# Kernel tuning notes

Measured on AMD Instinct MI355X. Metric: run time of the kernel, lower is better.

## Reference

```python
import jax, jax.numpy as jnp
import numpy as np

IN_DIM = 1024
MEM_DIM = 1024
T = 256
M = 512


def setup_inputs() -> dict:
    key = jax.random.key(0)
    ks = jax.random.split(key, 16)
    s = 0.02
    return {
        "inputs": jax.random.normal(ks[0], (T, 1, IN_DIM), jnp.float32),
        "hiddn_state_mat": jax.random.normal(ks[1], (M, MEM_DIM), jnp.float32),
        "W_ioux": jax.random.normal(ks[2], (IN_DIM, 3 * MEM_DIM), jnp.float32) * s,
        "b_ioux": jnp.zeros((3 * MEM_DIM,), jnp.float32),
        "W_iouh": jax.random.normal(ks[3], (MEM_DIM, 3 * MEM_DIM), jnp.float32) * s,
        "b_iouh": jnp.zeros((3 * MEM_DIM,), jnp.float32),
        "W_fx": jax.random.normal(ks[4], (IN_DIM, MEM_DIM), jnp.float32) * s,
        "b_fx": jnp.zeros((MEM_DIM,), jnp.float32),
        "W_fh": jax.random.normal(ks[5], (MEM_DIM, MEM_DIM), jnp.float32) * s,
        "b_fh": jnp.zeros((MEM_DIM,), jnp.float32),
        "Wa": jax.random.normal(ks[6], (1, MEM_DIM), jnp.float32) * 0.05,
        "W_attnh": jax.random.normal(ks[7], (2 * MEM_DIM, MEM_DIM), jnp.float32) * s,
        "b_attnh": jnp.zeros((MEM_DIM,), jnp.float32),
    }


def reference(inputs, hiddn_state_mat, W_ioux, b_ioux, W_iouh, b_iouh,
              W_fx, b_fx, W_fh, b_fh, Wa, W_attnh, b_attnh):
    m = W_fh.shape[1]
    n_rows = hiddn_state_mat.shape[0]

    def step(carry, x):
        c, h = carry  # [1, m] each; x: [1, in_dim]
        iou = x @ W_ioux + b_ioux + h @ W_iouh + b_iouh  # [1, 3m]
        i, o, u = jnp.split(iou, 3, axis=1)
        i = jax.nn.sigmoid(i); o = jax.nn.sigmoid(o); u = jnp.tanh(u)
        f = jax.nn.sigmoid(h @ W_fh + b_fh + x @ W_fx + b_fx)  # [1, m]
        c_new = i * u + f * c  # sum over the single child is identity
        h_new = o * jnp.tanh(c_new)  # [1, m]
        # attention over fixed hidden-state memory
        h_rep = jnp.broadcast_to(h_new, (n_rows, m))
        cat = jnp.concatenate([h_rep, hiddn_state_mat], axis=1)  # [M, 2m]
        t = jnp.tanh(cat @ W_attnh + b_attnh)  # [M, m]
        scores = t @ Wa[0]  # [M] == Wa @ t.T
        s = jax.nn.softmax(scores)[:, None]  # [M, 1]
        h_att = (jnp.sum((1.0 - s) * hiddn_state_mat, axis=0, keepdims=True)
                 + jnp.sum(s * h_rep, axis=0, keepdims=True))  # [1, m]
        return (c_new, h_att), h_att[0]

    init = (jnp.zeros((1, m), inputs.dtype), jnp.zeros((1, m), inputs.dtype))
    (_, _), h_all = jax.lax.scan(step, init, inputs)
    return h_all  # [T, mem_dim]; last row is the final child_h
```

## Files before the change

### kernel.cpp

```cpp
#include <hip/hip_runtime.h>
#include <hip/hip_bf16.h>

#define T_STEPS 256
#define MDIM 1024
#define MROWS 512
#define NBLK 128
#define GRID NBLK
#define NTHR 512

#define OFF_WGB     0u
#define OFF_WATT    2097152u
#define OFF_HPRET   3145728u
#define OFF_XIOU    3670016u
#define OFF_XF      4456448u
#define OFF_G       4718592u
#define OFF_HT      5767168u
#define OFF_HCOL    6291456u
#define OFF_HCOLW   6292480u
#define OFF_SCORED  6297600u
#define OFF_HLINE   6313984u

#define BIAS32  4294967296.0
#define SUBBIAS (16.0 * 4294967296.0)
#define DONE_TH (16.0 * 4294967296.0 - 1073741824.0)

typedef __attribute__((ext_vector_type(8))) short short8;
typedef __attribute__((ext_vector_type(4))) float f32x4;

__device__ inline float fast_tanh(float v) {
    float x = fminf(fmaxf(v, -15.f), 15.f);
    float z = __expf(2.f * x);
    return (z - 1.f) / (z + 1.f);
}
__device__ inline float sigm(float v) { return 1.f / (1.f + __expf(-v)); }

__device__ inline float wave_red(float v) {
#pragma unroll
    for (int s = 32; s > 0; s >>= 1) v += __shfl_down(v, s, 64);
    return v;
}

__device__ __host__ inline unsigned short f2b(float f) {
    __hip_bfloat16 h = __float2bfloat16(f);
    return *(unsigned short*)&h;
}
__device__ inline float b2f(unsigned short u) {
    union { unsigned i; float f; } v; v.i = ((unsigned)u) << 16; return v.f;
}

__device__ inline double gloadd(const double* p) {
    return __hip_atomic_load(p, __ATOMIC_RELAXED, __HIP_MEMORY_SCOPE_AGENT);
}
__device__ inline void gstored(double* p, double v) {
    __hip_atomic_store(p, v, __ATOMIC_RELAXED, __HIP_MEMORY_SCOPE_AGENT);
}
__device__ inline void gatomicd(double* p, double v) {
    __hip_atomic_fetch_add(p, v, __ATOMIC_RELAXED, __HIP_MEMORY_SCOPE_AGENT);
}
__device__ inline unsigned long long gloadu64(const unsigned long long* p) {
    return __hip_atomic_load(p, __ATOMIC_RELAXED, __HIP_MEMORY_SCOPE_AGENT);
}
__device__ inline void gstoreu64(unsigned long long* p, unsigned long long v) {
    __hip_atomic_store(p, v, __ATOMIC_RELAXED, __HIP_MEMORY_SCOPE_AGENT);
}


__global__ void build_wg(const float* __restrict__ Wiouh, const float* __restrict__ Wfh,
                         unsigned short* __restrict__ Wgb) {
    int k = blockIdx.y;
    int g = blockIdx.x * 256 + threadIdx.x;
    unsigned a = f2b(Wiouh[k * 3072 + g]);
    unsigned b = f2b(Wiouh[k * 3072 + 1024 + g]);
    unsigned c = f2b(Wiouh[k * 3072 + 2048 + g]);
    unsigned d = f2b(Wfh[k * 1024 + g]);
    uint2 p; p.x = a | (b << 16); p.y = c | (d << 16);
    *(uint2*)(Wgb + (size_t)k * 4096 + 4 * g) = p;
}

__global__ void transpose_g(const float* __restrict__ src, float* __restrict__ dst,
                            int R, int C) {
    __shared__ float tile[32][33];
    int c = blockIdx.x * 32 + threadIdx.x;
    int r0 = blockIdx.y * 32;
    for (int i = threadIdx.y; i < 32; i += 8)
        tile[i][threadIdx.x] = src[(size_t)(r0 + i) * C + c];
    __syncthreads();
    int r = r0 + threadIdx.x;
    int c0 = blockIdx.x * 32;
    for (int i = threadIdx.y; i < 32; i += 8)
        dst[(size_t)(c0 + i) * R + r] = tile[threadIdx.x][i];
}

__global__ __launch_bounds__(256) void mfma_gemm(
    const float* __restrict__ A, const float* __restrict__ B,
    const float* __restrict__ b1, const float* __restrict__ b2,
    float* __restrict__ C, unsigned short* __restrict__ Gb,
    int M, int N, int K, int tr, int cofs) {
    __shared__ unsigned short As[64 * 40];
    __shared__ unsigned short Bs[64 * 40];
    const int t = threadIdx.x;
    const int m0 = blockIdx.y * 64, n0 = blockIdx.x * 64;
    const int l = t & 63, w = t >> 6;
    const int fr = l & 15, fk = (l >> 4) * 8;
    const int ar = t >> 2, ak = (t & 3) * 8;
    const int bn = t >> 2, bk = (t & 3) * 8;
    f32x4 acc[4] = {};

    for (int kk = 0; kk < K; kk += 32) {
        const float4 a0 = *(const float4*)(A + (size_t)(m0 + ar) * K + kk + ak);
        const float4 a1 = *(const float4*)(A + (size_t)(m0 + ar) * K + kk + ak + 4);
        short8 av;
        av[0] = f2b(a0.x); av[1] = f2b(a0.y); av[2] = f2b(a0.z); av[3] = f2b(a0.w);
        av[4] = f2b(a1.x); av[5] = f2b(a1.y); av[6] = f2b(a1.z); av[7] = f2b(a1.w);
        short8 bv;
#pragma unroll
        for (int i = 0; i < 8; i++)
            bv[i] = f2b(B[(size_t)(kk + bk + i) * N + n0 + bn]);
        __syncthreads();
        *(short8*)(As + ar * 40 + ak) = av;
        *(short8*)(Bs + bn * 40 + bk) = bv;
        __syncthreads();
        const short8 af = *(const short8*)(As + (w * 16 + fr) * 40 + fk);
#pragma unroll
        for (int c = 0; c < 4; c++) {
            const short8 bf = *(const short8*)(Bs + (c * 16 + fr) * 40 + fk);
            acc[c] = __builtin_amdgcn_mfma_f32_16x16x32_bf16(af, bf, acc[c], 0, 0, 0);
        }
    }
#pragma unroll
    for (int c = 0; c < 4; c++) {
#pragma unroll
        for (int r = 0; r < 4; r++) {
            int m = m0 + w * 16 + (l >> 4) * 4 + r;
            int n = n0 + c * 16 + (l & 15);
            float v = acc[c][r];
            if (Gb) {
                int cp = 4 * (n & 1023) + (n >> 10) + cofs;
                Gb[(size_t)m * 4096 + cp] = f2b(v);
            } else {
                if (b1) v += b1[n];
                if (b2) v += b2[n];
                if (tr) C[(size_t)n * M + m] = v;
                else    C[(size_t)m * N + n] = v;
            }
        }
    }
}

__global__ void colsum_k(const float* __restrict__ H, float* __restrict__ out) {
    int k = blockIdx.x * 256 + threadIdx.x;
    float s = 0.f;
#pragma unroll 8
    for (int r = 0; r < MROWS; r++) s += H[(size_t)r * MDIM + k];
    out[k] = s;
}

__global__ void hcolw_k(const float* __restrict__ Hcol,
                        const unsigned short* __restrict__ Wgb,
                        float* __restrict__ HcolW) {
    int j = blockIdx.x * 256 + threadIdx.x;
    float acc = 0.f;
#pragma unroll 8
    for (int k = 0; k < 1024; k++)
        acc = fmaf(Hcol[k], b2f(Wgb[(size_t)k * 4096 + j]), acc);
    HcolW[j] = acc;
}

__device__ inline float sum8(const float* s) {
    return s[0] + s[1] + s[2] + s[3] + s[4] + s[5] + s[6] + s[7];
}

__global__ __launch_bounds__(NTHR, 2) void recurrent(
    const unsigned short* __restrict__ Wgb, const float* __restrict__ WatT,
    const float* __restrict__ HpreT, const float* __restrict__ HT,
    const float* __restrict__ Hcol, const float* __restrict__ HcolW,
    const unsigned short* __restrict__ Gb, const float* __restrict__ X_iou,
    const float* __restrict__ X_f, const float* __restrict__ Wa,
    unsigned long long* hline, double* scored, float* out) {

    const int b = blockIdx.x, t = threadIdx.x;
    const int x = b & 7, y = b >> 3;
    const int g_col = x * 128 + y * 8;
    const int j0 = x * 512 + y * 32;
    float creg = 0.f;
    __shared__ float smem[2648];
    float* hs   = smem;
    float* le   = smem + 1056;
    float* red  = smem + 1568;
    float* red2 = smem + 2080;
    float* sred = smem + 2592;
    float* sred2= smem + 2600;
    float* dotb = smem + 2608;
    float* attr = smem + 2640;

    const int jt = t & 31, kq = t >> 5;
    const int li = t & 63, tr = t >> 6;
    const int tl = t & 127, hi = t >> 7;

    float wregf[64];
#pragma unroll
    for (int i = 0; i < 64; i++)
        wregf[i] = b2f(Wgb[(size_t)(kq * 64 + i) * 4096 + j0 + jt]);
    float gregf[32];
#pragma unroll
    for (int i = 0; i < 32; i++)
        gregf[i] = b2f(Gb[(size_t)(kq * 32 + i) * 4096 + j0 + jt]);
    float watreg[16];
#pragma unroll
    for (int i = 0; i < 16; i++)
        watreg[i] = WatT[(size_t)(g_col + tr) * 1024 + i * 64 + li];
    float htr[8], hpr[8], wa8[8];
#pragma unroll
    for (int i = 0; i < 8; i++)
        htr[i] = HT[(size_t)(g_col + tr) * 512 + li + 64 * i];
#pragma unroll
    for (int c = 0; c < 8; c++) {
        hpr[c] = HpreT[(size_t)(g_col + c) * 512 + t];
        wa8[c] = Wa[g_col + c];
    }
    const float hcw   = (t < 32) ? HcolW[j0 + t] : 0.f;
    const float hcolg = (t < 8) ? Hcol[g_col + t] : 0.f;

    red[kq * 32 + jt] = 0.f;

    for (int st = 0; st < T_STEPS; st++) {
        float xi0 = 0.f, xi1 = 0.f, xi2 = 0.f, xf0 = 0.f;
        if (t < 8) {
            int g = g_col + t;
            xi0 = X_iou[(size_t)st * 3072 + g];
            xi1 = X_iou[(size_t)st * 3072 + 1024 + g];
            xi2 = X_iou[(size_t)st * 3072 + 2048 + g];
            xf0 = X_f[(size_t)st * 1024 + g];
        }
        float sc = 0.f;
        if (st > 0) {
            const double* sp = scored + (size_t)((st + 1) & 1) * 4096 + t;
            double vv[8];
            for (;;) {
                bool ok = true;
#pragma unroll
                for (int c = 0; c < 8; c++) {
                    vv[c] = gloadd(sp + c * 512);
                    ok = ok && (vv[c] > DONE_TH);
                }
                if (ok) break;
                __builtin_amdgcn_s_sleep(1);
            }
            double accd = 0.0;
#pragma unroll
            for (int c = 0; c < 8; c++) accd += (vv[c] - SUBBIAS);
            sc = (float)accd;
        }
        float evv = __expf(sc);
        le[t] = evv;
        float sv = wave_red(evv);
        if ((t & 63) == 0) sred[t >> 6] = sv;
        __syncthreads();
        float a2 = 0.f;
#pragma unroll
        for (int i = 0; i < 32; i++)
            a2 = fmaf(le[kq * 32 + i], gregf[i], a2);
        red2[kq * 32 + jt] = a2;
        float pp = 0.f;
#pragma unroll
        for (int i = 0; i < 8; i++)
            pp = fmaf(le[li + 64 * i], htr[i], pp);
        pp = wave_red(pp);
        if ((t & 63) == 0) sred2[t >> 6] = pp;
        __syncthreads();
        if (t < 32) {
            float s1 = 0.f, s2 = 0.f;
#pragma unroll
            for (int q = 0; q < 16; q++) { s1 += red[q * 32 + t]; s2 += red2[q * 32 + t]; }
            float S = sum8(sred);
            float invS = (st == 0) ? 0.f : 1.f / S;
            float hw = (st == 0) ? 0.f : hcw;
            dotb[t] = s1 + hw - invS * s2;
        }
        if (t < 8) {
            int g = g_col + t;
            if (st > 0) {
                float S = sum8(sred);
                float P = sred2[t];
                out[(size_t)(st - 1) * 1024 + g] =
                    hcolg + hs[g + (g >> 5)] - P / S;
            }
            float di = dotb[t * 4 + 0] + xi0;
            float doo = dotb[t * 4 + 1] + xi1;
            float du = dotb[t * 4 + 2] + xi2;
            float df = dotb[t * 4 + 3] + xf0;
            float ig = sigm(di), og = sigm(doo), fg = sigm(df);
            float ug = fast_tanh(du);
            creg = ig * ug + fg * creg;
            float hv = og * fast_tanh(creg);
            unsigned long long pkt =
                ((unsigned long long)(unsigned)(st + 1) << 32) | __float_as_uint(hv);
            gstoreu64(hline + (size_t)b * 8 + t, pkt);
        }
        __syncthreads();

        {
            const unsigned long long* lp = hline + (size_t)tl * 8 + hi * 2;
            const unsigned tgt = (unsigned)(st + 1);
            unsigned long long u0, u1;
            for (;;) {
                u0 = gloadu64(lp);
                u1 = gloadu64(lp + 1);
                if ((unsigned)(u0 >> 32) >= tgt && (unsigned)(u1 >> 32) >= tgt) break;
                __builtin_amdgcn_s_sleep(1);
            }
            int gc = (tl & 7) * 128 + (tl >> 3) * 8 + hi * 2;
            union { unsigned u; float f; } c0, c1;
            c0.u = (unsigned)u0; c1.u = (unsigned)u1;
            hs[gc + (gc >> 5)] = c0.f;
            int g1 = gc + 1; hs[g1 + (g1 >> 5)] = c1.f;
        }
        __syncthreads();
        if (t < 32)
            gstored(scored + (size_t)((st + 1) & 1) * 4096 + (size_t)b * 32 + t, 0.0);
        {
            float acc = 0.f;
#pragma unroll
            for (int i = 0; i < 16; i++) {
                int k = i * 64 + li;
                acc = fmaf(watreg[i], hs[k + (k >> 5)], acc);
            }
            acc = wave_red(acc);
            if ((t & 63) == 0) attr[t >> 6] = acc;
            __syncthreads();
            float ps = 0.f;
#pragma unroll
            for (int c = 0; c < 8; c++)
                ps = fmaf(wa8[c], fast_tanh(hpr[c] + attr[c]), ps);
            __asm__ volatile("" ::: "memory");
            __builtin_amdgcn_s_waitcnt(0);
            gatomicd(scored + (size_t)(st & 1) * 4096 + x * 512 + t,
                     (double)ps + BIAS32);
        }
        {
            float a = 0.f;
#pragma unroll
            for (int i = 0; i < 64; i++) {
                int k = kq * 64 + i;
                a = fmaf(hs[k + (k >> 5)], wregf[i], a);
            }
            red[kq * 32 + jt] = a;
        }
    }

    {
        const double* sp = scored + (size_t)((T_STEPS + 1) & 1) * 4096 + t;
        double vv[8];
        for (;;) {
            bool ok = true;
#pragma unroll
            for (int c = 0; c < 8; c++) {
                vv[c] = gloadd(sp + c * 512);
                ok = ok && (vv[c] > DONE_TH);
            }
            if (ok) break;
            __builtin_amdgcn_s_sleep(1);
        }
        double accd = 0.0;
#pragma unroll
        for (int c = 0; c < 8; c++) accd += (vv[c] - SUBBIAS);
        float evv = __expf((float)accd);
        le[t] = evv;
        float sv = wave_red(evv);
        if ((t & 63) == 0) sred[t >> 6] = sv;
        __syncthreads();
        float pp = 0.f;
#pragma unroll
        for (int i = 0; i < 8; i++)
            pp = fmaf(le[li + 64 * i], htr[i], pp);
        pp = wave_red(pp);
        if ((t & 63) == 0) sred2[t >> 6] = pp;
        __syncthreads();
        if (t < 8) {
            int g = g_col + t;
            float S = sum8(sred);
            float P = sred2[t];
            out[(size_t)(T_STEPS - 1) * 1024 + g] =
                hcolg + hs[g + (g >> 5)] - P / S;
        }
    }
}

extern "C" void kernel_launch(void* const* d_in, const int* in_sizes, int n_in,
                              void* d_out, int out_size, void* d_ws, size_t ws_size,
                              hipStream_t stream) {
    const float* inputs  = (const float*)d_in[0];
    const float* hiddn   = (const float*)d_in[1];
    const float* W_ioux  = (const float*)d_in[2];
    const float* b_ioux  = (const float*)d_in[3];
    const float* W_iouh  = (const float*)d_in[4];
    const float* b_iouh  = (const float*)d_in[5];
    const float* W_fx    = (const float*)d_in[6];
    const float* b_fx    = (const float*)d_in[7];
    const float* W_fh    = (const float*)d_in[8];
    const float* b_fh    = (const float*)d_in[9];
    const float* Wa      = (const float*)d_in[10];
    const float* W_attnh = (const float*)d_in[11];
    const float* b_attnh = (const float*)d_in[12];

    float* ws = (float*)d_ws;
    unsigned short* Wgb = (unsigned short*)(ws + OFF_WGB);
    float* WatT  = ws + OFF_WATT;
    float* HpreT = ws + OFF_HPRET;
    float* X_iou = ws + OFF_XIOU;
    float* X_f   = ws + OFF_XF;
    unsigned short* Gb = (unsigned short*)(ws + OFF_G);
    float* HT    = ws + OFF_HT;
    float* Hcol  = ws + OFF_HCOL;
    float* HcolW = ws + OFF_HCOLW;
    double* scored = (double*)(ws + OFF_SCORED);
    unsigned long long* hline = (unsigned long long*)(ws + OFF_HLINE);
    float* out   = (float*)d_out;

    hipMemsetAsync(ws + OFF_SCORED, 0, (16384 + 2048) * sizeof(float), stream);

    build_wg<<<dim3(4, 1024), 256, 0, stream>>>(W_iouh, W_fh, Wgb);
    transpose_g<<<dim3(32, 32), dim3(32, 8), 0, stream>>>(W_attnh, WatT, 1024, 1024);
    transpose_g<<<dim3(32, 16), dim3(32, 8), 0, stream>>>(hiddn, HT, 512, 1024);
    mfma_gemm<<<dim3(48, 4), 256, 0, stream>>>(inputs, W_ioux, b_ioux, b_iouh, X_iou, nullptr, 256, 3072, 1024, 0, 0);
    mfma_gemm<<<dim3(16, 4), 256, 0, stream>>>(inputs, W_fx, b_fx, b_fh, X_f, nullptr, 256, 1024, 1024, 0, 0);
    mfma_gemm<<<dim3(16, 8), 256, 0, stream>>>(hiddn, W_attnh + 1024 * 1024, b_attnh, nullptr, HpreT, nullptr, 512, 1024, 1024, 1, 0);
    colsum_k<<<4, 256, 0, stream>>>(hiddn, Hcol);
    hcolw_k<<<16, 256, 0, stream>>>(Hcol, Wgb, HcolW);
    mfma_gemm<<<dim3(48, 8), 256, 0, stream>>>(hiddn, W_iouh, nullptr, nullptr, nullptr, Gb, 512, 3072, 1024, 0, 0);
    mfma_gemm<<<dim3(16, 8), 256, 0, stream>>>(hiddn, W_fh, nullptr, nullptr, nullptr, Gb, 512, 1024, 1024, 0, 3);

    recurrent<<<GRID, NTHR, 0, stream>>>(Wgb, WatT, HpreT, HT, Hcol, HcolW, Gb,
                                         X_iou, X_f, Wa, hline, scored, out);
}
```

Before: 1.577 ms.

## Fuse precompute GEMMs, fold HcolW into recurrent kernel, spread score atomics

The five separate precompute GEMM launches become two: one for the input-side projections and one for the hidden-memory projections. The column-sum and HcolW kernels are removed; the column sum now reads the transposed matrix, and HcolW is computed inside the recurrent kernel from its register-resident weights. Score accumulation is spread over 16 slots instead of 8, which halves contention on each atomic target. In exchange, every step must poll twice as many doubles, and the double-buffer layout and memset size grow to match.

```diff
diff --git a/kernel.cpp b/kernel.cpp
--- a/kernel.cpp
+++ b/kernel.cpp
@@ -16,13 +16,12 @@
 #define OFF_G       4718592u
 #define OFF_HT      5767168u
 #define OFF_HCOL    6291456u
-#define OFF_HCOLW   6292480u
 #define OFF_SCORED  6297600u
-#define OFF_HLINE   6313984u
+#define OFF_HLINE   6330368u
 
 #define BIAS32  4294967296.0
-#define SUBBIAS (16.0 * 4294967296.0)
-#define DONE_TH (16.0 * 4294967296.0 - 1073741824.0)
+#define SUBBIAS (8.0 * 4294967296.0)
+#define DONE_TH (8.0 * 4294967296.0 - 1073741824.0)
 
 typedef __attribute__((ext_vector_type(8))) short short8;
 typedef __attribute__((ext_vector_type(4))) float f32x4;
@@ -91,79 +90,109 @@
         dst[(size_t)(c0 + i) * R + r] = tile[threadIdx.x][i];
 }
 
-__global__ __launch_bounds__(256) void mfma_gemm(
-    const float* __restrict__ A, const float* __restrict__ B,
-    const float* __restrict__ b1, const float* __restrict__ b2,
-    float* __restrict__ C, unsigned short* __restrict__ Gb,
-    int M, int N, int K, int tr, int cofs) {
+__global__ void colsum2_k(const float* __restrict__ HT, float* __restrict__ out) {
+    int k = blockIdx.x * 32 + (threadIdx.x >> 3);
+    int sub = threadIdx.x & 7;
+    const float* row = HT + (size_t)k * 512 + sub * 64;
+    float s = 0.f;
+#pragma unroll
+    for (int j = 0; j < 16; j++) {
+        float4 v = *(const float4*)(row + j * 4);
+        s += v.x + v.y + v.z + v.w;
+    }
+#pragma unroll
+    for (int d = 4; d > 0; d >>= 1) s += __shfl_down(s, d, 8);
+    if (sub == 0) out[k] = s;
+}
+
+#define MFMA_TILE_BODY(Bptr, LDB, NC0)                                         \
+    for (int kk = 0; kk < 1024; kk += 32) {                                    \
+        const float4 a0 = *(const float4*)(A + (size_t)(m0 + ar) * 1024 + kk + ak);      \
+        const float4 a1 = *(const float4*)(A + (size_t)(m0 + ar) * 1024 + kk + ak + 4);  \
+        short8 av;                                                             \
+        av[0] = f2b(a0.x); av[1] = f2b(a0.y); av[2] = f2b(a0.z); av[3] = f2b(a0.w); \
+        av[4] = f2b(a1.x); av[5] = f2b(a1.y); av[6] = f2b(a1.z); av[7] = f2b(a1.w); \
+        short8 bv;                                                             \
+        _Pragma("unroll")                                                      \
+        for (int i = 0; i < 8; i++)                                            \
+            bv[i] = f2b((Bptr)[(size_t)(kk + bk + i) * (LDB) + (NC0) + bn]);   \
+        __syncthreads();                                                       \
+        *(short8*)(As + ar * 40 + ak) = av;                                    \
+        *(short8*)(Bs + bn * 40 + bk) = bv;                                    \
+        __syncthreads();                                                       \
+        const short8 af = *(const short8*)(As + (w * 16 + fr) * 40 + fk);      \
+        _Pragma("unroll")                                                      \
+        for (int c = 0; c < 4; c++) {                                          \
+            const short8 bf = *(const short8*)(Bs + (c * 16 + fr) * 40 + fk);  \
+            acc[c] = __builtin_amdgcn_mfma_f32_16x16x32_bf16(af, bf, acc[c], 0, 0, 0); \
+        }                                                                      \
+    }
+
+__global__ __launch_bounds__(256) void gemm_x(
+    const float* __restrict__ A, const float* __restrict__ Wioux,
+    const float* __restrict__ Wfx, const float* __restrict__ bioux,
+    const float* __restrict__ biouh, const float* __restrict__ bfx,
+    const float* __restrict__ bfh, float* __restrict__ Xiou,
+    float* __restrict__ Xf) {
     __shared__ unsigned short As[64 * 40];
     __shared__ unsigned short Bs[64 * 40];
     const int t = threadIdx.x;
-    const int m0 = blockIdx.y * 64, n0 = blockIdx.x * 64;
+    const int n0g = blockIdx.x * 64, m0 = blockIdx.y * 64;
     const int l = t & 63, w = t >> 6;
     const int fr = l & 15, fk = (l >> 4) * 8;
     const int ar = t >> 2, ak = (t & 3) * 8;
     const int bn = t >> 2, bk = (t & 3) * 8;
+    const float* B; const float* c1; const float* c2; float* C;
+    int ldb, ldc, nc0;
+    if (n0g < 3072) { B = Wioux; ldb = 3072; nc0 = n0g; C = Xiou; ldc = 3072; c1 = bioux; c2 = biouh; }
+    else            { B = Wfx;   ldb = 1024; nc0 = n0g - 3072; C = Xf; ldc = 1024; c1 = bfx; c2 = bfh; }
     f32x4 acc[4] = {};
-
-    for (int kk = 0; kk < K; kk += 32) {
-        const float4 a0 = *(const float4*)(A + (size_t)(m0 + ar) * K + kk + ak);
-        const float4 a1 = *(const float4*)(A + (size_t)(m0 + ar) * K + kk + ak + 4);
-        short8 av;
-        av[0] = f2b(a0.x); av[1] = f2b(a0.y); av[2] = f2b(a0.z); av[3] = f2b(a0.w);
-        av[4] = f2b(a1.x); av[5] = f2b(a1.y); av[6] = f2b(a1.z); av[7] = f2b(a1.w);
-        short8 bv;
-#pragma unroll
-        for (int i = 0; i < 8; i++)
-            bv[i] = f2b(B[(size_t)(kk + bk + i) * N + n0 + bn]);
-        __syncthreads();
-        *(short8*)(As + ar * 40 + ak) = av;
-        *(short8*)(Bs + bn * 40 + bk) = bv;
-        __syncthreads();
-        const short8 af = *(const short8*)(As + (w * 16 + fr) * 40 + fk);
-#pragma unroll
-        for (int c = 0; c < 4; c++) {
-            const short8 bf = *(const short8*)(Bs + (c * 16 + fr) * 40 + fk);
-            acc[c] = __builtin_amdgcn_mfma_f32_16x16x32_bf16(af, bf, acc[c], 0, 0, 0);
-        }
-    }
-#pragma unroll
-    for (int c = 0; c < 4; c++) {
+    MFMA_TILE_BODY(B, ldb, nc0)
+#pragma unroll
+    for (int c = 0; c < 4; c++)
 #pragma unroll
         for (int r = 0; r < 4; r++) {
             int m = m0 + w * 16 + (l >> 4) * 4 + r;
-            int n = n0 + c * 16 + (l & 15);
+            int n = nc0 + c * 16 + (l & 15);
+            C[(size_t)m * ldc + n] = acc[c][r] + c1[n] + c2[n];
+        }
+}
+
+__global__ __launch_bounds__(256) void gemm_h(
+    const float* __restrict__ A, const float* __restrict__ Wiouh,
+    const float* __restrict__ Wfh, const float* __restrict__ Wat,
+    const float* __restrict__ battnh, unsigned short* __restrict__ Gb,
+    float* __restrict__ HpreT) {
+    __shared__ unsigned short As[64 * 40];
+    __shared__ unsigned short Bs[64 * 40];
+    const int t = threadIdx.x;
+    const int n0g = blockIdx.x * 64, m0 = blockIdx.y * 64;
+    const int l = t & 63, w = t >> 6;
+    const int fr = l & 15, fk = (l >> 4) * 8;
+    const int ar = t >> 2, ak = (t & 3) * 8;
+    const int bn = t >> 2, bk = (t & 3) * 8;
+    const float* B; int ldb, nc0, mode;
+    if (n0g < 3072)      { B = Wiouh; ldb = 3072; nc0 = n0g; mode = 0; }
+    else if (n0g < 4096) { B = Wfh;   ldb = 1024; nc0 = n0g - 3072; mode = 1; }
+    else                 { B = Wat;   ldb = 1024; nc0 = n0g - 4096; mode = 2; }
+    f32x4 acc[4] = {};
+    MFMA_TILE_BODY(B, ldb, nc0)
+#pragma unroll
+    for (int c = 0; c < 4; c++)
+#pragma unroll
+        for (int r = 0; r < 4; r++) {
+            int m = m0 + w * 16 + (l >> 4) * 4 + r;
+            int n = nc0 + c * 16 + (l & 15);
             float v = acc[c][r];
-            if (Gb) {
-                int cp = 4 * (n & 1023) + (n >> 10) + cofs;
+            if (mode == 0) {
+                int cp = 4 * (n & 1023) + (n >> 10);
                 Gb[(size_t)m * 4096 + cp] = f2b(v);
+            } else if (mode == 1) {
+                Gb[(size_t)m * 4096 + 4 * n + 3] = f2b(v);
             } else {
-                if (b1) v += b1[n];
-                if (b2) v += b2[n];
-                if (tr) C[(size_t)n * M + m] = v;
-                else    C[(size_t)m * N + n] = v;
-            }
-        }
-    }
-}
-
-__global__ void colsum_k(const float* __restrict__ H, float* __restrict__ out) {
-    int k = blockIdx.x * 256 + threadIdx.x;
-    float s = 0.f;
-#pragma unroll 8
-    for (int r = 0; r < MROWS; r++) s += H[(size_t)r * MDIM + k];
-    out[k] = s;
-}
-
-__global__ void hcolw_k(const float* __restrict__ Hcol,
-                        const unsigned short* __restrict__ Wgb,
-                        float* __restrict__ HcolW) {
-    int j = blockIdx.x * 256 + threadIdx.x;
-    float acc = 0.f;
-#pragma unroll 8
-    for (int k = 0; k < 1024; k++)
-        acc = fmaf(Hcol[k], b2f(Wgb[(size_t)k * 4096 + j]), acc);
-    HcolW[j] = acc;
+                HpreT[(size_t)n * 512 + m] = v + battnh[n];
+            }
+        }
 }
 
 __device__ inline float sum8(const float* s) {
@@ -173,15 +202,16 @@
 __global__ __launch_bounds__(NTHR, 2) void recurrent(
     const unsigned short* __restrict__ Wgb, const float* __restrict__ WatT,
     const float* __restrict__ HpreT, const float* __restrict__ HT,
-    const float* __restrict__ Hcol, const float* __restrict__ HcolW,
-    const unsigned short* __restrict__ Gb, const float* __restrict__ X_iou,
-    const float* __restrict__ X_f, const float* __restrict__ Wa,
+    const float* __restrict__ Hcol, const unsigned short* __restrict__ Gb,
+    const float* __restrict__ X_iou, const float* __restrict__ X_f,
+    const float* __restrict__ Wa,
     unsigned long long* hline, double* scored, float* out) {
 
     const int b = blockIdx.x, t = threadIdx.x;
     const int x = b & 7, y = b >> 3;
     const int g_col = x * 128 + y * 8;
     const int j0 = x * 512 + y * 32;
+    const int cidx = x * 2 + (y & 1);
     float creg = 0.f;
     __shared__ float smem[2648];
     float* hs   = smem;
@@ -218,9 +248,27 @@
         hpr[c] = HpreT[(size_t)(g_col + c) * 512 + t];
         wa8[c] = Wa[g_col + c];
     }
-    const float hcw   = (t < 32) ? HcolW[j0 + t] : 0.f;
     const float hcolg = (t < 8) ? Hcol[g_col + t] : 0.f;
 
+    hs[t + (t >> 5)] = Hcol[t];
+    { int k2 = t + 512; hs[k2 + (k2 >> 5)] = Hcol[t + 512]; }
+    __syncthreads();
+    {
+        float hp = 0.f;
+#pragma unroll
+        for (int i = 0; i < 64; i++) {
+            int k = kq * 64 + i;
+            hp = fmaf(hs[k + (k >> 5)], wregf[i], hp);
+        }
+        red[kq * 32 + jt] = hp;
+    }
+    __syncthreads();
+    float hcw = 0.f;
+    if (t < 32) {
+#pragma unroll
+        for (int q = 0; q < 16; q++) hcw += red[q * 32 + t];
+    }
+    __syncthreads();
     red[kq * 32 + jt] = 0.f;
 
     for (int st = 0; st < T_STEPS; st++) {
@@ -234,12 +282,12 @@
         }
         float sc = 0.f;
         if (st > 0) {
-            const double* sp = scored + (size_t)((st + 1) & 1) * 4096 + t;
-            double vv[8];
+            const double* sp = scored + (size_t)((st + 1) & 1) * 8192 + t;
+            double vv[16];
             for (;;) {
                 bool ok = true;
 #pragma unroll
-                for (int c = 0; c < 8; c++) {
+                for (int c = 0; c < 16; c++) {
                     vv[c] = gloadd(sp + c * 512);
                     ok = ok && (vv[c] > DONE_TH);
                 }
@@ -248,7 +296,7 @@
             }
             double accd = 0.0;
 #pragma unroll
-            for (int c = 0; c < 8; c++) accd += (vv[c] - SUBBIAS);
+            for (int c = 0; c < 16; c++) accd += (vv[c] - SUBBIAS);
             sc = (float)accd;
         }
         float evv = __expf(sc);
@@ -316,8 +364,8 @@
             int g1 = gc + 1; hs[g1 + (g1 >> 5)] = c1.f;
         }
         __syncthreads();
-        if (t < 32)
-            gstored(scored + (size_t)((st + 1) & 1) * 4096 + (size_t)b * 32 + t, 0.0);
+        if (t < 64)
+            gstored(scored + (size_t)((st + 1) & 1) * 8192 + (size_t)b * 64 + t, 0.0);
         {
             float acc = 0.f;
 #pragma unroll
@@ -334,7 +382,7 @@
                 ps = fmaf(wa8[c], fast_tanh(hpr[c] + attr[c]), ps);
             __asm__ volatile("" ::: "memory");
             __builtin_amdgcn_s_waitcnt(0);
-            gatomicd(scored + (size_t)(st & 1) * 4096 + x * 512 + t,
+            gatomicd(scored + (size_t)(st & 1) * 8192 + (size_t)cidx * 512 + t,
                      (double)ps + BIAS32);
         }
         {
@@ -349,12 +397,12 @@
     }
 
     {
-        const double* sp = scored + (size_t)((T_STEPS + 1) & 1) * 4096 + t;
-        double vv[8];
+        const double* sp = scored + (size_t)((T_STEPS + 1) & 1) * 8192 + t;
+        double vv[16];
         for (;;) {
             bool ok = true;
 #pragma unroll
-            for (int c = 0; c < 8; c++) {
+            for (int c = 0; c < 16; c++) {
                 vv[c] = gloadd(sp + c * 512);
                 ok = ok && (vv[c] > DONE_TH);
             }
@@ -363,7 +411,7 @@
         }
         double accd = 0.0;
 #pragma unroll
-        for (int c = 0; c < 8; c++) accd += (vv[c] - SUBBIAS);
+        for (int c = 0; c < 16; c++) accd += (vv[c] - SUBBIAS);
         float evv = __expf((float)accd);
         le[t] = evv;
         float sv = wave_red(evv);
@@ -412,24 +460,21 @@
     unsigned short* Gb = (unsigned short*)(ws + OFF_G);
     float* HT    = ws + OFF_HT;
     float* Hcol  = ws + OFF_HCOL;
-    float* HcolW = ws + OFF_HCOLW;
     double* scored = (double*)(ws + OFF_SCORED);
     unsigned long long* hline = (unsigned long long*)(ws + OFF_HLINE);
     float* out   = (float*)d_out;
 
-    hipMemsetAsync(ws + OFF_SCORED, 0, (16384 + 2048) * sizeof(float), stream);
+    hipMemsetAsync(ws + OFF_SCORED, 0, (32768 + 2048) * sizeof(float), stream);
 
     build_wg<<<dim3(4, 1024), 256, 0, stream>>>(W_iouh, W_fh, Wgb);
     transpose_g<<<dim3(32, 32), dim3(32, 8), 0, stream>>>(W_attnh, WatT, 1024, 1024);
     transpose_g<<<dim3(32, 16), dim3(32, 8), 0, stream>>>(hiddn, HT, 512, 1024);
-    mfma_gemm<<<dim3(48, 4), 256, 0, stream>>>(inputs, W_ioux, b_ioux, b_iouh, X_iou, nullptr, 256, 3072, 1024, 0, 0);
-    mfma_gemm<<<dim3(16, 4), 256, 0, stream>>>(inputs, W_fx, b_fx, b_fh, X_f, nullptr, 256, 1024, 1024, 0, 0);
-    mfma_gemm<<<dim3(16, 8), 256, 0, stream>>>(hiddn, W_attnh + 1024 * 1024, b_attnh, nullptr, HpreT, nullptr, 512, 1024, 1024, 1, 0);
-    colsum_k<<<4, 256, 0, stream>>>(hiddn, Hcol);
-    hcolw_k<<<16, 256, 0, stream>>>(Hcol, Wgb, HcolW);
-    mfma_gemm<<<dim3(48, 8), 256, 0, stream>>>(hiddn, W_iouh, nullptr, nullptr, nullptr, Gb, 512, 3072, 1024, 0, 0);
-    mfma_gemm<<<dim3(16, 8), 256, 0, stream>>>(hiddn, W_fh, nullptr, nullptr, nullptr, Gb, 512, 1024, 1024, 0, 3);
-
-    recurrent<<<GRID, NTHR, 0, stream>>>(Wgb, WatT, HpreT, HT, Hcol, HcolW, Gb,
+    colsum2_k<<<32, 256, 0, stream>>>(HT, Hcol);
+    gemm_x<<<dim3(64, 4), 256, 0, stream>>>(inputs, W_ioux, W_fx, b_ioux, b_iouh,
+                                            b_fx, b_fh, X_iou, X_f);
+    gemm_h<<<dim3(80, 8), 256, 0, stream>>>(hiddn, W_iouh, W_fh,
+                                            W_attnh + 1024 * 1024, b_attnh, Gb, HpreT);
+
+    recurrent<<<GRID, NTHR, 0, stream>>>(Wgb, WatT, HpreT, HT, Hcol, Gb,
                                          X_iou, X_f, Wa, hline, scored, out);
 }
```

After: 1.606 ms. About the same (+1.8%).
